# Kernel optimization log

Measured on AMD Instinct MI355X. Metric: run time of the kernel, lower is better.

The kernel has to match this reference:

```python
import jax, jax.numpy as jnp
import numpy as np
import math

B, NQ, NK = 32, 1024, 1024
DQ = DK = DV = 512
H = 8
EPS = 1e-5


def _layernorm(x, g, b):
    mu = jnp.mean(x, axis=-1, keepdims=True)
    var = jnp.mean(jnp.square(x - mu), axis=-1, keepdims=True)
    return (x - mu) * jax.lax.rsqrt(var + EPS) * g + b


def setup_inputs() -> dict:
    key = jax.random.key(0)
    ks = jax.random.split(key, 8)
    s = 0.03  # small init scale for linear weights
    return {
        "Q": jax.random.normal(ks[0], (B, NQ, DQ), jnp.float32),
        "K": jax.random.normal(ks[1], (B, NK, DK), jnp.float32),
        "Wq": jax.random.normal(ks[2], (DQ, DV), jnp.float32) * s,
        "bq": jnp.zeros((DV,), jnp.float32),
        "Wk": jax.random.normal(ks[3], (DK, DV), jnp.float32) * s,
        "bk": jnp.zeros((DV,), jnp.float32),
        "Wv": jax.random.normal(ks[4], (DK, DV), jnp.float32) * s,
        "bv": jnp.zeros((DV,), jnp.float32),
        "Wo": jax.random.normal(ks[5], (DV, DV), jnp.float32) * s,
        "bo": jnp.zeros((DV,), jnp.float32),
        "g0": jnp.ones((DV,), jnp.float32),
        "beta0": jnp.zeros((DV,), jnp.float32),
        "g1": jnp.ones((DV,), jnp.float32),
        "beta1": jnp.zeros((DV,), jnp.float32),
    }


def reference(Q, K, Wq, bq, Wk, bk, Wv, bv, Wo, bo, g0, beta0, g1, beta1):
    b, nq, _ = Q.shape
    nk = K.shape[1]
    d = DV // H  # head dim (dim_split)

    q = Q @ Wq + bq            # [B, Nq, DV]
    k = K @ Wk + bk            # [B, Nk, DV]
    v = K @ Wv + bv            # [B, Nk, DV]

    # torch.cat(x.split(d, 2), 0) == reshape to [B,N,H,d] then stack heads on batch dim
    qh = q.reshape(b, nq, H, d).transpose(2, 0, 1, 3)  # [H, B, Nq, d]
    kh = k.reshape(b, nk, H, d).transpose(2, 0, 1, 3)  # [H, B, Nk, d]
    vh = v.reshape(b, nk, H, d).transpose(2, 0, 1, 3)  # [H, B, Nk, d]

    # NOTE: scaled by sqrt(dim_V), and softmax over the QUERY axis (torch dim=1)
    scores = jnp.einsum('hbqd,hbkd->hbqk', qh, kh) / math.sqrt(DV)
    A = jax.nn.softmax(scores, axis=2)                 # over Nq (faithful to source)
    oh = qh + jnp.einsum('hbqk,hbkd->hbqd', A, vh)     # residual on Q_

    out = oh.transpose(1, 2, 0, 3).reshape(b, nq, DV)  # merge heads back
    out = _layernorm(out, g0, beta0)
    out = out + jax.nn.relu(out @ Wo + bo)
    out = _layernorm(out, g1, beta1)
    return out
```

## Files before the change

kernel.cpp:

```cpp
#include <hip/hip_runtime.h>

#define Bz  32
#define NQz 1024
#define NKz 1024
#define SCALE 0.04419417382415922f

typedef __bf16 bf16_t;
typedef bf16_t bf16x8 __attribute__((ext_vector_type(8)));
typedef bf16_t bf16x4 __attribute__((ext_vector_type(4)));
typedef float  f32x4  __attribute__((ext_vector_type(4)));

#define MFMA16(a, b, c) __builtin_amdgcn_mfma_f32_16x16x32_bf16(a, b, c, 0, 0, 0)

#define SBAR() asm volatile("s_barrier" ::: "memory")
#define WAITVM(n) asm volatile("s_waitcnt vmcnt(" #n ")" ::: "memory")
#define WAITVL(n) asm volatile("s_waitcnt vmcnt(" #n ") lgkmcnt(0)" ::: "memory")

__device__ __forceinline__ void gll16(const void* g, void* l) {
  __builtin_amdgcn_global_load_lds(
      (const __attribute__((address_space(1))) void*)g,
      (__attribute__((address_space(3))) void*)l, 16, 0, 0);
}

__device__ __forceinline__ float fexp2(float x) {
#if __has_builtin(__builtin_amdgcn_exp2f)
  return __builtin_amdgcn_exp2f(x);
#else
  float r;
  asm("v_exp_f32 %0, %1" : "=v"(r) : "v"(x));
  return r;
#endif
}

__device__ __forceinline__ bf16x8 cvt8(float4 a, float4 b) {
  bf16x8 r;
  r[0] = (bf16_t)a.x; r[1] = (bf16_t)a.y; r[2] = (bf16_t)a.z; r[3] = (bf16_t)a.w;
  r[4] = (bf16_t)b.x; r[5] = (bf16_t)b.y; r[6] = (bf16_t)b.z; r[7] = (bf16_t)b.w;
  return r;
}

__global__ void transpose_w(const float* __restrict__ W0, const float* __restrict__ W1,
                            const float* __restrict__ W2, const float* __restrict__ W3,
                            bf16_t* __restrict__ out) {
  __shared__ float tile[32][33];
  const float* W = blockIdx.z == 0 ? W0 : blockIdx.z == 1 ? W1 : blockIdx.z == 2 ? W2 : W3;
  bf16_t* o = out + (size_t)blockIdx.z * 512 * 512;
  const int n0 = blockIdx.x * 32, k0 = blockIdx.y * 32;
  const int tx = threadIdx.x, ty = threadIdx.y;
  for (int i = 0; i < 4; i++)
    tile[ty + i * 8][tx] = W[(size_t)(k0 + ty + i * 8) * 512 + n0 + tx];
  __syncthreads();
  for (int i = 0; i < 4; i++)
    o[(size_t)(n0 + ty + i * 8) * 512 + k0 + tx] = (bf16_t)tile[tx][ty + i * 8];
}

template <int DUAL>
__global__ __launch_bounds__(256) void gemm_f32a(const float* __restrict__ A,
                                                 const bf16_t* __restrict__ Wt,
                                                 const float* __restrict__ b0v,
                                                 const float* __restrict__ b1v,
                                                 float mult0,
                                                 bf16_t* __restrict__ C0,
                                                 bf16_t* __restrict__ C1) {
  __shared__ __align__(16) bf16_t As[128][40];
  __shared__ __align__(16) bf16_t Bs[2][128 * 32];
  const int t = threadIdx.x;
  const int wave = t >> 6, lane = t & 63;
  const int quad = lane >> 4, l16 = lane & 15;
  const int wm = wave & 1, wn = wave >> 1;
  const int m0 = blockIdx.x * 128, n0 = blockIdx.y * 128;
  const int r = t >> 1, half = t & 1;
  const int drow = lane >> 2;
  const int dg = (lane & 3) ^ ((lane >> 3) & 3);

  f32x4 acc[4][4] = {};

  const float* arow = A + (size_t)(m0 + r) * 512 + half * 16;
  const bf16_t* wrow = Wt + (size_t)(n0 + wave * 16 + drow) * 512 + dg * 8;

  for (int p = 0; p < 2; p++)
    gll16(wrow + (size_t)(p * 64) * 512, &Bs[0][(p * 256 + wave * 64) * 8]);
  float4 a0 = *(const float4*)(arow + 0);
  float4 a1 = *(const float4*)(arow + 4);
  float4 a2 = *(const float4*)(arow + 8);
  float4 a3 = *(const float4*)(arow + 12);

  for (int it = 0; it < 16; it++) {
    const int cur = it & 1;
    if (it < 15)
      for (int p = 0; p < 2; p++)
        gll16(wrow + (it + 1) * 32 + (size_t)(p * 64) * 512,
              &Bs[cur ^ 1][(p * 256 + wave * 64) * 8]);
    *(bf16x8*)&As[r][half * 16 + 0] = cvt8(a0, a1);
    *(bf16x8*)&As[r][half * 16 + 8] = cvt8(a2, a3);
    if (it < 15) {
      const float* ap = arow + (it + 1) * 32;
      a0 = *(const float4*)(ap + 0);
      a1 = *(const float4*)(ap + 4);
      a2 = *(const float4*)(ap + 8);
      a3 = *(const float4*)(ap + 12);
      WAITVL(6);
    } else {
      WAITVL(0);
    }
    SBAR();
    bf16x8 af[4], bfv[4];
    for (int mt = 0; mt < 4; mt++)
      af[mt] = *(const bf16x8*)&As[wm * 64 + mt * 16 + l16][quad * 8];
    for (int nt = 0; nt < 4; nt++) {
      const int rB = wn * 64 + nt * 16 + l16;
      bfv[nt] = *(const bf16x8*)&Bs[cur][rB * 32 + ((quad ^ ((rB >> 1) & 3)) * 8)];
    }
    for (int mt = 0; mt < 4; mt++)
      for (int nt = 0; nt < 4; nt++)
        acc[mt][nt] = MFMA16(af[mt], bfv[nt], acc[mt][nt]);
    SBAR();
  }

  const float* bias = (!DUAL || n0 < 512) ? b0v : b1v;
  bf16_t* C = (!DUAL || n0 < 512) ? C0 : C1;
  const float mult = (!DUAL || n0 < 512) ? mult0 : 1.0f;
  const int nb = (!DUAL || n0 < 512) ? n0 : n0 - 512;
  for (int mt = 0; mt < 4; mt++) {
    for (int nt = 0; nt < 4; nt++) {
      const int row = m0 + wm * 64 + mt * 16 + quad * 4;
      const int col = nb + wn * 64 + nt * 16 + l16;
      const float bv = bias[col];
      for (int rg = 0; rg < 4; rg++)
        C[(size_t)(row + rg) * 512 + col] = (bf16_t)((acc[mt][nt][rg] + bv) * mult);
    }
  }
}

__global__ __launch_bounds__(256) void gemm_bf16a(const bf16_t* __restrict__ A,
                                                  const bf16_t* __restrict__ Wt,
                                                  const float* __restrict__ bias,
                                                  bf16_t* __restrict__ C) {
  __shared__ __align__(16) bf16_t As[128][40];
  __shared__ __align__(16) bf16_t Bs[2][128 * 32];
  const int t = threadIdx.x;
  const int wave = t >> 6, lane = t & 63;
  const int quad = lane >> 4, l16 = lane & 15;
  const int wm = wave & 1, wn = wave >> 1;
  const int m0 = blockIdx.x * 128, n0 = blockIdx.y * 128;
  const int r = t >> 1, half = t & 1;
  const int drow = lane >> 2;
  const int dg = (lane & 3) ^ ((lane >> 3) & 3);

  f32x4 acc[4][4] = {};

  const bf16_t* arow = A + (size_t)(m0 + r) * 512 + half * 16;
  const bf16_t* wrow = Wt + (size_t)(n0 + wave * 16 + drow) * 512 + dg * 8;

  for (int p = 0; p < 2; p++)
    gll16(wrow + (size_t)(p * 64) * 512, &Bs[0][(p * 256 + wave * 64) * 8]);
  bf16x8 v0 = *(const bf16x8*)(arow + 0);
  bf16x8 v1 = *(const bf16x8*)(arow + 8);

  for (int it = 0; it < 16; it++) {
    const int cur = it & 1;
    if (it < 15)
      for (int p = 0; p < 2; p++)
        gll16(wrow + (it + 1) * 32 + (size_t)(p * 64) * 512,
              &Bs[cur ^ 1][(p * 256 + wave * 64) * 8]);
    *(bf16x8*)&As[r][half * 16 + 0] = v0;
    *(bf16x8*)&As[r][half * 16 + 8] = v1;
    if (it < 15) {
      const bf16_t* ap = arow + (it + 1) * 32;
      v0 = *(const bf16x8*)(ap + 0);
      v1 = *(const bf16x8*)(ap + 8);
      WAITVL(4);
    } else {
      WAITVL(0);
    }
    SBAR();
    bf16x8 af[4], bfv[4];
    for (int mt = 0; mt < 4; mt++)
      af[mt] = *(const bf16x8*)&As[wm * 64 + mt * 16 + l16][quad * 8];
    for (int nt = 0; nt < 4; nt++) {
      const int rB = wn * 64 + nt * 16 + l16;
      bfv[nt] = *(const bf16x8*)&Bs[cur][rB * 32 + ((quad ^ ((rB >> 1) & 3)) * 8)];
    }
    for (int mt = 0; mt < 4; mt++)
      for (int nt = 0; nt < 4; nt++)
        acc[mt][nt] = MFMA16(af[mt], bfv[nt], acc[mt][nt]);
    SBAR();
  }

  for (int mt = 0; mt < 4; mt++) {
    for (int nt = 0; nt < 4; nt++) {
      const int row = m0 + wm * 64 + mt * 16 + quad * 4;
      const int col = n0 + wn * 64 + nt * 16 + l16;
      const float bv = bias[col];
      for (int rg = 0; rg < 4; rg++) {
        float v = acc[mt][nt][rg] + bv;
        float x = (float)A[(size_t)(row + rg) * 512 + col];
        C[(size_t)(row + rg) * 512 + col] = (bf16_t)(x + fmaxf(v, 0.f));
      }
    }
  }
}

__global__ __launch_bounds__(256) void attn_stats(const bf16_t* __restrict__ qp,
                                                  const bf16_t* __restrict__ kp,
                                                  const bf16_t* __restrict__ vp,
                                                  bf16_t* __restrict__ Vt) {
  __shared__ __align__(16) bf16_t Vs[128][72];
  __shared__ __align__(16) bf16_t Qs[2][64 * 64];
  __shared__ float ls[128];
  const int t = threadIdx.x;
  const int wave = t >> 6, lane = t & 63;
  const int quad = lane >> 4, l16 = lane & 15;
  const int id = blockIdx.x;
  const int kb = ((id >> 3) & 7) * 128;
  const int hb = (id & 7) * 32 + (id >> 6);
  const int h = hb >> 5, b = hb & 31;
  const bf16_t* qbase = qp + (size_t)b * NQz * 512 + h * 64;
  const bf16_t* kbase = kp + (size_t)b * NKz * 512 + h * 64;
  const int drow = lane >> 3;
  const int dg = (lane & 7) ^ drow;

  {
    const int r = t >> 1, half = t & 1;
    const bf16_t* vr = vp + (size_t)b * NKz * 512 + (size_t)(kb + r) * 512 + h * 64 + half * 32;
    *(bf16x8*)&Vs[r][half * 32 + 0]  = *(const bf16x8*)(vr + 0);
    *(bf16x8*)&Vs[r][half * 32 + 8]  = *(const bf16x8*)(vr + 8);
    *(bf16x8*)&Vs[r][half * 32 + 16] = *(const bf16x8*)(vr + 16);
    *(bf16x8*)&Vs[r][half * 32 + 24] = *(const bf16x8*)(vr + 24);
  }

  bf16x8 aK[2][2];
  for (int mt = 0; mt < 2; mt++) {
    const bf16_t* kr = kbase + (size_t)(kb + wave * 32 + mt * 16 + l16) * 512 + quad * 8;
    aK[mt][0] = *(const bf16x8*)kr;
    aK[mt][1] = *(const bf16x8*)(kr + 32);
  }

  for (int p = 0; p < 2; p++) {
    const bf16_t* src = qbase + (size_t)(p * 32 + wave * 8 + drow) * 512 + dg * 8;
    gll16(src, &Qs[0][(p * 256 + wave * 64) * 8]);
  }

  const f32x4 fz = {0.f, 0.f, 0.f, 0.f};
  f32x4 lacc[2] = {};
  for (int it = 0; it < 16; it++) {
    const int cur = it & 1;
    WAITVM(0);
    SBAR();
    if (it < 15) {
      const int qn = (it + 1) * 64;
      for (int p = 0; p < 2; p++) {
        const bf16_t* src = qbase + (size_t)(qn + p * 32 + wave * 8 + drow) * 512 + dg * 8;
        gll16(src, &Qs[cur ^ 1][(p * 256 + wave * 64) * 8]);
      }
    }
    for (int nt = 0; nt < 4; nt++) {
      const int rQ = nt * 16 + l16;
      bf16x8 b0 = *(const bf16x8*)&Qs[cur][rQ * 64 + ((quad ^ (rQ & 7)) * 8)];
      bf16x8 b1 = *(const bf16x8*)&Qs[cur][rQ * 64 + (((quad + 4) ^ (rQ & 7)) * 8)];
      for (int mt = 0; mt < 2; mt++) {
        f32x4 s = MFMA16(aK[mt][0], b0, fz);
        s = MFMA16(aK[mt][1], b1, s);
        lacc[mt][0] += fexp2(s[0]);
        lacc[mt][1] += fexp2(s[1]);
        lacc[mt][2] += fexp2(s[2]);
        lacc[mt][3] += fexp2(s[3]);
      }
    }
  }
  for (int mt = 0; mt < 2; mt++) {
    for (int rg = 0; rg < 4; rg++) {
      float v = lacc[mt][rg];
      v += __shfl_xor(v, 1);
      v += __shfl_xor(v, 2);
      v += __shfl_xor(v, 4);
      v += __shfl_xor(v, 8);
      if (l16 == 0) ls[wave * 32 + mt * 16 + quad * 4 + rg] = 1.0f / v;
    }
  }
  __syncthreads();
  const int d = t >> 2, kc = (t & 3) * 32;
  bf16_t* vtr = Vt + (size_t)hb * 64 * 1024 + (size_t)d * 1024 + kb + kc;
  for (int c = 0; c < 4; c++) {
    bf16x8 o;
    for (int j = 0; j < 8; j++)
      o[j] = (bf16_t)((float)Vs[kc + c * 8 + j][d] * ls[kc + c * 8 + j]);
    *(bf16x8*)(vtr + c * 8) = o;
  }
}

__global__ __launch_bounds__(256) void attn_out(const bf16_t* __restrict__ qp,
                                                const bf16_t* __restrict__ kp,
                                                const bf16_t* __restrict__ Vt,
                                                bf16_t* __restrict__ oh) {
  __shared__ __align__(16) bf16_t Ks[2][64 * 64];
  __shared__ __align__(16) bf16_t Vts[2][64 * 64];
  __shared__ __align__(16) bf16_t Ps[128][72];
  const int t = threadIdx.x;
  const int wave = t >> 6, lane = t & 63;
  const int quad = lane >> 4, l16 = lane & 15;
  const int id = blockIdx.x;
  const int qt = (id >> 3) & 7;
  const int hb = (id & 7) * 32 + (id >> 6);
  const int h = hb >> 5, b = hb & 31;
  const int q0 = qt * 128;
  const bf16_t* qbase = qp + (size_t)b * NQz * 512 + h * 64;
  const bf16_t* kbase = kp + (size_t)b * NKz * 512 + h * 64;
  const bf16_t* vtbase = Vt + (size_t)hb * 64 * 1024;
  const int drow = lane >> 3;
  const int dg = (lane & 7) ^ drow;

  bf16x8 bQ[2][2];
  for (int nt = 0; nt < 2; nt++) {
    const bf16_t* qr = qbase + (size_t)(q0 + wave * 32 + nt * 16 + l16) * 512 + quad * 8;
    bQ[nt][0] = *(const bf16x8*)qr;
    bQ[nt][1] = *(const bf16x8*)(qr + 32);
  }

  for (int p = 0; p < 2; p++) {
    const bf16_t* ksrc = kbase + (size_t)(p * 32 + wave * 8 + drow) * 512 + dg * 8;
    gll16(ksrc, &Ks[0][(p * 256 + wave * 64) * 8]);
    const bf16_t* vsrc = vtbase + (size_t)(p * 32 + wave * 8 + drow) * 1024 + dg * 8;
    gll16(vsrc, &Vts[0][(p * 256 + wave * 64) * 8]);
  }

  const f32x4 fz = {0.f, 0.f, 0.f, 0.f};
  f32x4 acc[2][4] = {};
  for (int it = 0; it < 16; it++) {
    const int kk = it * 64;
    const int cur = it & 1;
    WAITVM(0);
    SBAR();
    if (it < 15) {
      const int kn = kk + 64;
      for (int p = 0; p < 2; p++) {
        const bf16_t* ksrc = kbase + (size_t)(kn + p * 32 + wave * 8 + drow) * 512 + dg * 8;
        gll16(ksrc, &Ks[cur ^ 1][(p * 256 + wave * 64) * 8]);
        const bf16_t* vsrc = vtbase + (size_t)(p * 32 + wave * 8 + drow) * 1024 + kn + dg * 8;
        gll16(vsrc, &Vts[cur ^ 1][(p * 256 + wave * 64) * 8]);
      }
    }
    for (int mt = 0; mt < 4; mt++) {
      const int rK = mt * 16 + l16;
      bf16x8 a0 = *(const bf16x8*)&Ks[cur][rK * 64 + ((quad ^ (rK & 7)) * 8)];
      bf16x8 a1 = *(const bf16x8*)&Ks[cur][rK * 64 + (((quad + 4) ^ (rK & 7)) * 8)];
      for (int nt = 0; nt < 2; nt++) {
        f32x4 s = MFMA16(a0, bQ[nt][0], fz);
        s = MFMA16(a1, bQ[nt][1], s);
        bf16x4 pk;
        pk[0] = (bf16_t)fexp2(s[0]);
        pk[1] = (bf16_t)fexp2(s[1]);
        pk[2] = (bf16_t)fexp2(s[2]);
        pk[3] = (bf16_t)fexp2(s[3]);
        *(bf16x4*)&Ps[wave * 32 + nt * 16 + l16][mt * 16 + quad * 4] = pk;
      }
    }
    bf16x8 aP[2][2];
    for (int mt = 0; mt < 2; mt++) {
      aP[mt][0] = *(const bf16x8*)&Ps[wave * 32 + mt * 16 + l16][quad * 8];
      aP[mt][1] = *(const bf16x8*)&Ps[wave * 32 + mt * 16 + l16][quad * 8 + 32];
    }
    for (int nd = 0; nd < 4; nd++) {
      const int rV = nd * 16 + l16;
      bf16x8 b0 = *(const bf16x8*)&Vts[cur][rV * 64 + ((quad ^ (rV & 7)) * 8)];
      bf16x8 b1 = *(const bf16x8*)&Vts[cur][rV * 64 + (((quad + 4) ^ (rV & 7)) * 8)];
      for (int mt = 0; mt < 2; mt++) {
        acc[mt][nd] = MFMA16(aP[mt][0], b0, acc[mt][nd]);
        acc[mt][nd] = MFMA16(aP[mt][1], b1, acc[mt][nd]);
      }
    }
  }
  for (int mt = 0; mt < 2; mt++)
    for (int nd = 0; nd < 4; nd++)
      for (int rg = 0; rg < 4; rg++)
        Ps[wave * 32 + mt * 16 + quad * 4 + rg][nd * 16 + l16] = (bf16_t)acc[mt][nd][rg];
  const int row = wave * 32 + (lane >> 1), cc = (lane & 1) * 32;
  bf16_t* orow = oh + ((size_t)b * NQz + q0 + row) * 512 + h * 64 + cc;
  for (int c = 0; c < 4; c++)
    *(bf16x8*)(orow + c * 8) = *(const bf16x8*)&Ps[row][cc + c * 8];
}

template <int RES, int F32OUT>
__global__ __launch_bounds__(256) void ln_k(const bf16_t* __restrict__ x,
                                            const bf16_t* __restrict__ res,
                                            const float* __restrict__ g,
                                            const float* __restrict__ be,
                                            bf16_t* __restrict__ yb,
                                            float* __restrict__ yf) {
  const int wave = threadIdx.x >> 6, lane = threadIdx.x & 63;
  const size_t row = (size_t)blockIdx.x * 4 + wave;
  bf16x8 xv = *(const bf16x8*)(x + row * 512 + lane * 8);
  float xf[8];
  for (int i = 0; i < 8; i++) xf[i] = (float)xv[i];
  if (RES) {
    bf16x8 rv = *(const bf16x8*)(res + row * 512 + lane * 8);
    for (int i = 0; i < 8; i++) xf[i] += (float)rv[i];
  }
  float s = 0.f, sq = 0.f;
  for (int i = 0; i < 8; i++) { s += xf[i]; sq += xf[i] * xf[i]; }
  for (int off = 1; off < 64; off <<= 1) {
    s += __shfl_xor(s, off);
    sq += __shfl_xor(sq, off);
  }
  const float mu = s * (1.0f / 512.0f);
  const float var = sq * (1.0f / 512.0f) - mu * mu;
  const float rstd = rsqrtf(var + 1e-5f);
  float4 gv0 = *(const float4*)(g + lane * 8);
  float4 gv1 = *(const float4*)(g + lane * 8 + 4);
  float4 bv0 = *(const float4*)(be + lane * 8);
  float4 bv1 = *(const float4*)(be + lane * 8 + 4);
  float gg[8] = {gv0.x, gv0.y, gv0.z, gv0.w, gv1.x, gv1.y, gv1.z, gv1.w};
  float bb[8] = {bv0.x, bv0.y, bv0.z, bv0.w, bv1.x, bv1.y, bv1.z, bv1.w};
  float o[8];
  for (int i = 0; i < 8; i++) o[i] = (xf[i] - mu) * rstd * gg[i] + bb[i];
  if (F32OUT) {
    float4 o0 = {o[0], o[1], o[2], o[3]}, o1 = {o[4], o[5], o[6], o[7]};
    *(float4*)(yf + row * 512 + lane * 8) = o0;
    *(float4*)(yf + row * 512 + lane * 8 + 4) = o1;
  } else {
    bf16x8 ov;
    for (int i = 0; i < 8; i++) ov[i] = (bf16_t)o[i];
    *(bf16x8*)(yb + row * 512 + lane * 8) = ov;
  }
}

extern "C" void kernel_launch(void* const* d_in, const int* in_sizes, int n_in,
                              void* d_out, int out_size, void* d_ws, size_t ws_size,
                              hipStream_t stream) {
  (void)in_sizes; (void)n_in; (void)out_size; (void)ws_size;
  const float* Q   = (const float*)d_in[0];
  const float* K   = (const float*)d_in[1];
  const float* Wq  = (const float*)d_in[2];
  const float* bq  = (const float*)d_in[3];
  const float* Wk  = (const float*)d_in[4];
  const float* bk  = (const float*)d_in[5];
  const float* Wv  = (const float*)d_in[6];
  const float* bv  = (const float*)d_in[7];
  const float* Wo  = (const float*)d_in[8];
  const float* bo  = (const float*)d_in[9];
  const float* g0  = (const float*)d_in[10];
  const float* be0 = (const float*)d_in[11];
  const float* g1  = (const float*)d_in[12];
  const float* be1 = (const float*)d_in[13];
  float* outp = (float*)d_out;

  char* w = (char*)d_ws;
  bf16_t* Wt  = (bf16_t*)w;
  bf16_t* qp  = (bf16_t*)(w + (2ull << 20));
  bf16_t* kp  = (bf16_t*)(w + (34ull << 20));
  bf16_t* vp  = (bf16_t*)(w + (66ull << 20));
  bf16_t* Vt  = (bf16_t*)(w + (98ull << 20));
  bf16_t* ohb = (bf16_t*)(w + (130ull << 20));
  bf16_t* x0b = vp;
  bf16_t* oh2 = kp;

  transpose_w<<<dim3(16, 16, 4), dim3(32, 8), 0, stream>>>(Wq, Wk, Wv, Wo, Wt);
  gemm_f32a<0><<<dim3(256, 4), 256, 0, stream>>>(Q, Wt, bq, nullptr, 1.0f, qp, nullptr);
  gemm_f32a<1><<<dim3(256, 8), 256, 0, stream>>>(K, Wt + (1 << 18), bk, bv,
                                                 SCALE * 1.4426950408889634f, kp, vp);
  attn_stats<<<2048, 256, 0, stream>>>(qp, kp, vp, Vt);
  attn_out<<<2048, 256, 0, stream>>>(qp, kp, Vt, ohb);
  ln_k<1, 0><<<8192, 256, 0, stream>>>(ohb, qp, g0, be0, x0b, nullptr);
  gemm_bf16a<<<dim3(256, 4), 256, 0, stream>>>(x0b, Wt + 3 * (1 << 18), bo, oh2);
  ln_k<0, 1><<<8192, 256, 0, stream>>>(oh2, nullptr, g1, be1, nullptr, outp);
}
```

Baseline: 493.7 us.

## Restructure attn_out into 512-thread blocks with 256-query tiles and 32-key steps

```diff
diff --git a/kernel.cpp b/kernel.cpp
--- a/kernel.cpp
+++ b/kernel.cpp
@@ -289,26 +289,24 @@
   }
 }
 
-__global__ __launch_bounds__(256) void attn_out(const bf16_t* __restrict__ qp,
-                                                const bf16_t* __restrict__ kp,
-                                                const bf16_t* __restrict__ Vt,
-                                                bf16_t* __restrict__ oh) {
-  __shared__ __align__(16) bf16_t Ks[2][64 * 64];
-  __shared__ __align__(16) bf16_t Vts[2][64 * 64];
-  __shared__ __align__(16) bf16_t Ps[128][72];
+__global__ __launch_bounds__(512, 6) void attn_out(const bf16_t* __restrict__ qp,
+                                                   const bf16_t* __restrict__ kp,
+                                                   const bf16_t* __restrict__ Vt,
+                                                   bf16_t* __restrict__ oh) {
+  __shared__ __align__(16) bf16_t pool[18432];
   const int t = threadIdx.x;
   const int wave = t >> 6, lane = t & 63;
   const int quad = lane >> 4, l16 = lane & 15;
   const int id = blockIdx.x;
-  const int qt = (id >> 3) & 7;
-  const int hb = (id & 7) * 32 + (id >> 6);
+  const int qt = (id >> 3) & 3;
+  const int hb = (id & 7) * 32 + (id >> 5);
   const int h = hb >> 5, b = hb & 31;
-  const int q0 = qt * 128;
+  const int q0 = qt * 256;
   const bf16_t* qbase = qp + (size_t)b * NQz * 512 + h * 64;
   const bf16_t* kbase = kp + (size_t)b * NKz * 512 + h * 64;
   const bf16_t* vtbase = Vt + (size_t)hb * 64 * 1024;
-  const int drow = lane >> 3;
-  const int dg = (lane & 7) ^ drow;
+
+  bf16_t* const Ps = pool + 8192;
 
   bf16x8 bQ[2][2];
   for (int nt = 0; nt < 2; nt++) {
@@ -317,33 +315,37 @@
     bQ[nt][1] = *(const bf16x8*)(qr + 32);
   }
 
-  for (int p = 0; p < 2; p++) {
-    const bf16_t* ksrc = kbase + (size_t)(p * 32 + wave * 8 + drow) * 512 + dg * 8;
-    gll16(ksrc, &Ks[0][(p * 256 + wave * 64) * 8]);
-    const bf16_t* vsrc = vtbase + (size_t)(p * 32 + wave * 8 + drow) * 1024 + dg * 8;
-    gll16(vsrc, &Vts[0][(p * 256 + wave * 64) * 8]);
-  }
+  const bool stK = wave < 4;
+  const int w4 = wave & 3;
+  const int kdrow = w4 * 8 + (lane >> 3);
+  const int kdg = (lane & 7) ^ (lane >> 3);
+  const int vdrow = w4 * 16 + (lane >> 2);
+  const int vdg = (lane & 3) ^ ((lane >> 2) & 3);
+
+  if (stK) gll16(kbase + (size_t)kdrow * 512 + kdg * 8, pool + w4 * 512);
+  else     gll16(vtbase + (size_t)vdrow * 1024 + vdg * 8, pool + 4096 + w4 * 512);
 
   const f32x4 fz = {0.f, 0.f, 0.f, 0.f};
   f32x4 acc[2][4] = {};
-  for (int it = 0; it < 16; it++) {
-    const int kk = it * 64;
+  for (int it = 0; it < 32; it++) {
     const int cur = it & 1;
-    WAITVM(0);
-    SBAR();
-    if (it < 15) {
-      const int kn = kk + 64;
-      for (int p = 0; p < 2; p++) {
-        const bf16_t* ksrc = kbase + (size_t)(kn + p * 32 + wave * 8 + drow) * 512 + dg * 8;
-        gll16(ksrc, &Ks[cur ^ 1][(p * 256 + wave * 64) * 8]);
-        const bf16_t* vsrc = vtbase + (size_t)(p * 32 + wave * 8 + drow) * 1024 + kn + dg * 8;
-        gll16(vsrc, &Vts[cur ^ 1][(p * 256 + wave * 64) * 8]);
-      }
-    }
-    for (int mt = 0; mt < 4; mt++) {
+    const bf16_t* const Ksc  = pool + cur * 2048;
+    const bf16_t* const Vtsc = pool + 4096 + cur * 2048;
+    if (it < 31) {
+      const int kn = (it + 1) * 32;
+      bf16_t* const Ksn  = pool + (cur ^ 1) * 2048;
+      bf16_t* const Vtsn = pool + 4096 + (cur ^ 1) * 2048;
+      if (stK) gll16(kbase + (size_t)(kn + kdrow) * 512 + kdg * 8, Ksn + w4 * 512);
+      else     gll16(vtbase + (size_t)vdrow * 1024 + kn + vdg * 8, Vtsn + w4 * 512);
+      WAITVM(1);
+    } else {
+      WAITVM(0);
+    }
+    SBAR();
+    for (int mt = 0; mt < 2; mt++) {
       const int rK = mt * 16 + l16;
-      bf16x8 a0 = *(const bf16x8*)&Ks[cur][rK * 64 + ((quad ^ (rK & 7)) * 8)];
-      bf16x8 a1 = *(const bf16x8*)&Ks[cur][rK * 64 + (((quad + 4) ^ (rK & 7)) * 8)];
+      bf16x8 a0 = *(const bf16x8*)&Ksc[rK * 64 + ((quad ^ (rK & 7)) * 8)];
+      bf16x8 a1 = *(const bf16x8*)&Ksc[rK * 64 + (((quad + 4) ^ (rK & 7)) * 8)];
       for (int nt = 0; nt < 2; nt++) {
         f32x4 s = MFMA16(a0, bQ[nt][0], fz);
         s = MFMA16(a1, bQ[nt][1], s);
@@ -352,32 +354,31 @@
         pk[1] = (bf16_t)fexp2(s[1]);
         pk[2] = (bf16_t)fexp2(s[2]);
         pk[3] = (bf16_t)fexp2(s[3]);
-        *(bf16x4*)&Ps[wave * 32 + nt * 16 + l16][mt * 16 + quad * 4] = pk;
+        *(bf16x4*)&Ps[(wave * 32 + nt * 16 + l16) * 40 + mt * 16 + quad * 4] = pk;
       }
     }
-    bf16x8 aP[2][2];
-    for (int mt = 0; mt < 2; mt++) {
-      aP[mt][0] = *(const bf16x8*)&Ps[wave * 32 + mt * 16 + l16][quad * 8];
-      aP[mt][1] = *(const bf16x8*)&Ps[wave * 32 + mt * 16 + l16][quad * 8 + 32];
-    }
+    bf16x8 aP[2];
+    for (int mt = 0; mt < 2; mt++)
+      aP[mt] = *(const bf16x8*)&Ps[(wave * 32 + mt * 16 + l16) * 40 + quad * 8];
     for (int nd = 0; nd < 4; nd++) {
       const int rV = nd * 16 + l16;
-      bf16x8 b0 = *(const bf16x8*)&Vts[cur][rV * 64 + ((quad ^ (rV & 7)) * 8)];
-      bf16x8 b1 = *(const bf16x8*)&Vts[cur][rV * 64 + (((quad + 4) ^ (rV & 7)) * 8)];
-      for (int mt = 0; mt < 2; mt++) {
-        acc[mt][nd] = MFMA16(aP[mt][0], b0, acc[mt][nd]);
-        acc[mt][nd] = MFMA16(aP[mt][1], b1, acc[mt][nd]);
-      }
-    }
-  }
+      bf16x8 bv = *(const bf16x8*)&Vtsc[rV * 32 + ((quad ^ (rV & 3)) * 8)];
+      acc[0][nd] = MFMA16(aP[0], bv, acc[0][nd]);
+      acc[1][nd] = MFMA16(aP[1], bv, acc[1][nd]);
+    }
+    SBAR();
+  }
+  bf16_t* Ob = pool;
   for (int mt = 0; mt < 2; mt++)
     for (int nd = 0; nd < 4; nd++)
       for (int rg = 0; rg < 4; rg++)
-        Ps[wave * 32 + mt * 16 + quad * 4 + rg][nd * 16 + l16] = (bf16_t)acc[mt][nd][rg];
+        Ob[(wave * 32 + mt * 16 + quad * 4 + rg) * 72 + nd * 16 + l16] =
+            (bf16_t)acc[mt][nd][rg];
+  __syncthreads();
   const int row = wave * 32 + (lane >> 1), cc = (lane & 1) * 32;
   bf16_t* orow = oh + ((size_t)b * NQz + q0 + row) * 512 + h * 64 + cc;
   for (int c = 0; c < 4; c++)
-    *(bf16x8*)(orow + c * 8) = *(const bf16x8*)&Ps[row][cc + c * 8];
+    *(bf16x8*)(orow + c * 8) = *(const bf16x8*)&Ob[row * 72 + cc + c * 8];
 }
 
 template <int RES, int F32OUT>
@@ -459,7 +460,7 @@
   gemm_f32a<1><<<dim3(256, 8), 256, 0, stream>>>(K, Wt + (1 << 18), bk, bv,
                                                  SCALE * 1.4426950408889634f, kp, vp);
   attn_stats<<<2048, 256, 0, stream>>>(qp, kp, vp, Vt);
-  attn_out<<<2048, 256, 0, stream>>>(qp, kp, Vt, ohb);
+  attn_out<<<1024, 512, 0, stream>>>(qp, kp, Vt, ohb);
   ln_k<1, 0><<<8192, 256, 0, stream>>>(ohb, qp, g0, be0, x0b, nullptr);
   gemm_bf16a<<<dim3(256, 4), 256, 0, stream>>>(x0b, Wt + 3 * (1 << 18), bo, oh2);
   ln_k<0, 1><<<8192, 256, 0, stream>>>(oh2, nullptr, g1, be1, nullptr, outp);
```

New measurement: 478.6 us. 3.1% less time.
